# Optimization experiments

Hardware: AMD Instinct MI355X
Metric: run time of the kernel (lower is better)

The kernel has to match this reference:

```python
import jax, jax.numpy as jnp
import numpy as np

B, L = 1024, 256
POOL, FM, HEAD, EMB = 4, 64, 64, 48  # input_size=256, pool_size=4 -> 64x64 maps


def _smooth(x, scale):
    # replicate-pad box filter of width 2*scale+1, via cumsum (single pass)
    w = 2 * scale + 1
    xp = jnp.pad(x, ((0, 0), (scale, scale)), mode='edge')          # (B, L+2s)
    c = jnp.pad(jnp.cumsum(xp, axis=1), ((0, 0), (1, 0)))           # (B, L+2s+1)
    return (c[:, w:] - c[:, :-w]) / w                               # (B, L)


def _picker(g, wmap, wbias, fcw, fcb):
    # g: (B, 256, 256) pairwise feature map
    b = g.shape[0]
    p = g.reshape(b, FM, POOL, FM, POOL).mean(axis=(2, 4))          # AvgPool2d(4): (B,64,64)
    h = jax.nn.elu(jnp.einsum('bij,hij->bh', p, wmap) + wbias)      # (B, head)
    return jax.nn.elu(h @ fcw.T + fcb)                              # (B, emb)


def setup_inputs() -> dict:
    key = jax.random.key(0)
    ks = jax.random.split(key, 16)
    x = jax.random.uniform(ks[0], (B, L), dtype=jnp.float32)
    d = {'x': x}
    for i, name in enumerate(['di', 'ndi', 'dd']):
        d[f'wm_{name}'] = jax.random.normal(ks[1 + 4 * i], (HEAD, FM, FM), jnp.float32)
        d[f'b_{name}'] = jax.random.normal(ks[2 + 4 * i], (HEAD,), jnp.float32)
        d[f'fcw_{name}'] = jax.random.normal(ks[3 + 4 * i], (EMB, HEAD), jnp.float32) * (1.0 / np.sqrt(HEAD))
        d[f'fcb_{name}'] = jax.random.normal(ks[4 + 4 * i], (EMB,), jnp.float32) * 0.01
    d['fc1_w'] = jax.random.normal(ks[13], (48, 3 * EMB), jnp.float32) * (1.0 / np.sqrt(3 * EMB))
    d['fc1_b'] = jax.random.normal(ks[14], (48,), jnp.float32) * 0.01
    d['fc2_w'] = jax.random.normal(ks[15], (20, 48), jnp.float32) * (1.0 / np.sqrt(48))
    d['fc2_b'] = jnp.zeros((20,), jnp.float32)
    return d


def reference(x, wm_di, b_di, fcw_di, fcb_di,
              wm_ndi, b_ndi, fcw_ndi, fcb_ndi,
              wm_dd, b_dd, fcw_dd, fcb_dd,
              fc1_w, fc1_b, fc2_w, fc2_b):
    sm = _smooth(x, 2)
    diff = jnp.diff(sm, axis=1, prepend=x[:, :1])                   # (B, L)
    xi, xj = x[:, :, None], x[:, None, :]
    DI = xj - xi                                                    # (B, L, L)
    NDI = DI / (xj + xi + 1e-5)
    DD = diff[:, None, :] - diff[:, :, None]
    e_di = _picker(DI, wm_di, b_di, fcw_di, fcb_di)
    e_ndi = _picker(NDI, wm_ndi, b_ndi, fcw_ndi, fcb_ndi)
    e_dd = _picker(DD, wm_dd, b_dd, fcw_dd, fcb_dd)
    emb = jnp.concatenate([e_di, e_ndi, e_dd], axis=1)              # (B, 144)
    emb = jax.nn.elu(emb @ fc1_w.T + fc1_b)
    return emb @ fc2_w.T + fc2_b                                    # (B, 20)
```

## Files before the change

kernel.cpp:

```cpp
#include <hip/hip_runtime.h>
#include <hip/hip_bf16.h>
#include <math.h>

typedef __attribute__((ext_vector_type(8))) short short8;
typedef __attribute__((ext_vector_type(4))) float floatx4;

#define WS_WREDT 0u
#define WS_WMAT  (1u << 20)

__device__ __forceinline__ float eluf(float v) {
  return v > 0.f ? v : __expf(v) - 1.f;
}

__device__ __forceinline__ unsigned short f2bf(float f) {
  __hip_bfloat16 h = __float2bfloat16(f);
  return *reinterpret_cast<unsigned short*>(&h);
}

__global__ __launch_bounds__(256) void prep_kernel(
    const float* __restrict__ wm_di,
    const float* __restrict__ wm_ndi,
    const float* __restrict__ wm_dd,
    char* __restrict__ ws) {
  __shared__ float sm[64 * 65];
  const int t = threadIdx.x;
  if (blockIdx.x < 128) {
    const int sel = blockIdx.x >> 6, h = blockIdx.x & 63;
    const float* w = (sel ? wm_dd : wm_di) + h * 4096;
#pragma unroll 4
    for (int i = 0; i < 16; ++i) {
      const int e = i * 256 + t;
      sm[(e >> 6) * 65 + (e & 63)] = w[e];
    }
    __syncthreads();
    if (t < 64) {
      float cs = 0.f, rs = 0.f;
#pragma unroll 8
      for (int I = 0; I < 64; ++I) {
        cs += sm[I * 65 + t];
        rs += sm[t * 65 + I];
      }
      ((float*)(ws + WS_WREDT))[sel * 4096 + t * 64 + h] = cs - rs;
    }
  } else {
    const int h = blockIdx.x - 128;
    const float* w = wm_ndi + h * 4096;
#pragma unroll 4
    for (int i = 0; i < 16; ++i) {
      const int e = i * 256 + t;
      sm[(e >> 6) * 65 + (e & 63)] = w[e];
    }
    __syncthreads();
    const int kstep = t >> 2, kc = t & 3;
    const int lane = kc * 16 + (h & 15);
    const int n = h >> 4;
    short8 sv;
#pragma unroll
    for (int j = 0; j < 8; ++j) {
      const int k = kstep * 32 + kc * 8 + j;
      const int I = k >> 5, tt = k & 31;
      const int J = (I + 1 + tt) & 63;
      float v = 0.f;
      if (!(tt == 31 && I >= 32))
        v = 0.0625f * (sm[I * 65 + J] - sm[J * 65 + I]);
      sv[j] = (short)f2bf(v);
    }
    *(short8*)((__hip_bfloat16*)(ws + WS_WMAT) + (((n * 64 + kstep) * 64 + lane) << 3)) = sv;
  }
}

__global__ __launch_bounds__(1024, 8) void fused_kernel(
    const float* __restrict__ x,
    const float* __restrict__ b_di, const float* __restrict__ b_ndi,
    const float* __restrict__ b_dd,
    const float* __restrict__ fcw_di, const float* __restrict__ fcb_di,
    const float* __restrict__ fcw_ndi, const float* __restrict__ fcb_ndi,
    const float* __restrict__ fcw_dd, const float* __restrict__ fcb_dd,
    const float* __restrict__ fc1_w, const float* __restrict__ fc1_b,
    const float* __restrict__ fc2_w, const float* __restrict__ fc2_b,
    const char* __restrict__ ws,
    float* __restrict__ out) {
  __shared__ float xs[2][256];
  __shared__ __align__(16) unsigned short ldsA[2][2][2048];
  __shared__ float pxs[2][64], pds[2][64];
  __shared__ float hp[16][4][2][16];
  __shared__ float hh[3][2][64];
  __shared__ float emb_s[2][144];
  __shared__ float f1v_s[2][48];

  const int t = threadIdx.x;
  const int b0 = blockIdx.x * 2;
  const float* __restrict__ wredT = (const float*)(ws + WS_WREDT);
  const short* __restrict__ wmaT = (const short*)(ws + WS_WMAT);

  if (t < 512) xs[t >> 8][t & 255] = x[(b0 + (t >> 8)) * 256 + (t & 255)];
  __syncthreads();

  if (t < 128) {
    const int r = t >> 6, m = t & 63;
    const float* __restrict__ xr = xs[r];
    const int b4 = 4 * m;
    pxs[r][m] = 0.25f * (xr[b4] + xr[b4 + 1] + xr[b4 + 2] + xr[b4 + 3]);
    const int i3 = min(b4 + 4, 255), i4 = min(b4 + 5, 255);
    const float smv = 0.2f * (xr[b4 + 1] + xr[b4 + 2] + xr[b4 + 3] + xr[i3] + xr[i4]);
    float prev = __shfl_up(smv, 1, 64);
    if (m == 0) prev = xr[0];
    pds[r][m] = 0.25f * (smv - prev);
  }

#pragma unroll 1
  for (int i = 0; i < 4; ++i) {
    const int cc = t + i * 1024;
    const int r = cc >> 11, e = cc & 2047;
    const int I = e >> 5;
    const int J = (I + 1 + (e & 31)) & 63;
    const float4 xiv = *(const float4*)&xs[r][I << 2];
    const float4 xjv = *(const float4*)&xs[r][J << 2];
    const float P01 = 2.f * xjv.x * xjv.y + (xjv.x + xjv.y) * 1e-5f;
    const float P23 = 2.f * xjv.z * xjv.w + (xjv.z + xjv.w) * 1e-5f;
    const float ya[4] = {xiv.x, xiv.y, xiv.z, xiv.w};
    float s = 0.f;
#pragma unroll
    for (int a = 0; a < 4; ++a) {
      const float y = ya[a];
      const float u = y + 1e-5f;
      const float G = 2.f * y * u;
      const float D0 = (xjv.x + u) * (xjv.y + u);
      const float D1 = (xjv.z + u) * (xjv.w + u);
      s += (P01 - G) * __builtin_amdgcn_rcpf(D0);
      s += (P23 - G) * __builtin_amdgcn_rcpf(D1);
    }
    const unsigned short hi = f2bf(s);
    union { unsigned int uu; float f; } hv; hv.uu = ((unsigned int)hi) << 16;
    ldsA[0][r][e] = hi;
    ldsA[1][r][e] = f2bf(s - hv.f);
  }
  __syncthreads();

  {
    const int kh = t >> 6, lane = t & 63;
    const int arow = lane & 1;
    const int kofs = kh * 128 + ((lane >> 4) << 3);
#pragma unroll
    for (int n = 0; n < 4; ++n) {
      floatx4 acc = {0.f, 0.f, 0.f, 0.f};
#pragma unroll
      for (int s = 0; s < 4; ++s) {
        const int kk = kofs + s * 32;
        const short8 ah = *(const short8*)&ldsA[0][arow][kk];
        const short8 al = *(const short8*)&ldsA[1][arow][kk];
        const int kstep = kh * 4 + s;
        const short8 bv = *(const short8*)(wmaT + (((n * 64 + kstep) * 64 + lane) << 3));
        acc = __builtin_amdgcn_mfma_f32_16x16x32_bf16(ah, bv, acc, 0, 0, 0);
        acc = __builtin_amdgcn_mfma_f32_16x16x32_bf16(al, bv, acc, 0, 0, 0);
      }
      if (lane < 16) {
        hp[kh][n][0][lane] = acc[0];
        hp[kh][n][1][lane] = acc[1];
      }
    }
  }

  if (t < 128) {
    const int r = t >> 6, h = t & 63;
    float adi = b_di[h], add_ = b_dd[h];
#pragma unroll 8
    for (int K = 0; K < 64; ++K) {
      adi += pxs[r][K] * wredT[K * 64 + h];
      add_ += pds[r][K] * wredT[4096 + K * 64 + h];
    }
    hh[0][r][h] = eluf(adi);
    hh[2][r][h] = eluf(add_);
  }
  __syncthreads();

  if (t < 128) {
    const int row = t >> 6, h = t & 63;
    const int n = h >> 4, c = h & 15;
    float v = b_ndi[h];
#pragma unroll
    for (int kh = 0; kh < 16; ++kh) v += hp[kh][n][row][c];
    hh[1][row][h] = eluf(v);
  }
  __syncthreads();

  if (t < 2 * 144) {
    const int r = t / 144;
    const int k = t - r * 144;
    const int pick = k / 48;
    const int e = k - pick * 48;
    const float* __restrict__ fw = (pick == 0) ? fcw_di : (pick == 1) ? fcw_ndi : fcw_dd;
    const float* __restrict__ fb = (pick == 0) ? fcb_di : (pick == 1) ? fcb_ndi : fcb_dd;
    float a = fb[e];
#pragma unroll 8
    for (int hq = 0; hq < 64; ++hq) a += hh[pick][r][hq] * fw[e * 64 + hq];
    emb_s[r][k] = eluf(a);
  }
  __syncthreads();

  if (t < 2 * 48) {
    const int r = t / 48, o = t - (t / 48) * 48;
    float a = fc1_b[o];
#pragma unroll 8
    for (int k = 0; k < 144; ++k) a += emb_s[r][k] * fc1_w[o * 144 + k];
    f1v_s[r][o] = eluf(a);
  }
  __syncthreads();

  if (t < 2 * 20) {
    const int r = t / 20, o = t - (t / 20) * 20;
    float a = fc2_b[o];
#pragma unroll
    for (int j = 0; j < 48; ++j) a += f1v_s[r][j] * fc2_w[o * 48 + j];
    out[(b0 + r) * 20 + o] = a;
  }
}

extern "C" void kernel_launch(void* const* d_in, const int* in_sizes, int n_in,
                              void* d_out, int out_size, void* d_ws, size_t ws_size,
                              hipStream_t stream) {
  const float* x       = (const float*)d_in[0];
  const float* wm_di   = (const float*)d_in[1];
  const float* b_di    = (const float*)d_in[2];
  const float* fcw_di  = (const float*)d_in[3];
  const float* fcb_di  = (const float*)d_in[4];
  const float* wm_ndi  = (const float*)d_in[5];
  const float* b_ndi   = (const float*)d_in[6];
  const float* fcw_ndi = (const float*)d_in[7];
  const float* fcb_ndi = (const float*)d_in[8];
  const float* wm_dd   = (const float*)d_in[9];
  const float* b_dd    = (const float*)d_in[10];
  const float* fcw_dd  = (const float*)d_in[11];
  const float* fcb_dd  = (const float*)d_in[12];
  const float* fc1_w   = (const float*)d_in[13];
  const float* fc1_b   = (const float*)d_in[14];
  const float* fc2_w   = (const float*)d_in[15];
  const float* fc2_b   = (const float*)d_in[16];
  float* out = (float*)d_out;
  char* ws = (char*)d_ws;

  prep_kernel<<<192, 256, 0, stream>>>(wm_di, wm_ndi, wm_dd, ws);
  fused_kernel<<<512, 1024, 0, stream>>>(
      x, b_di, b_ndi, b_dd,
      fcw_di, fcb_di, fcw_ndi, fcb_ndi, fcw_dd, fcb_dd,
      fc1_w, fc1_b, fc2_w, fc2_b, ws, out);
}
```

Before: 27.04 us.

## Fuse weight prep into main kernel with per-group flag synchronization

```diff
diff --git a/kernel.cpp b/kernel.cpp
--- a/kernel.cpp
+++ b/kernel.cpp
@@ -5,8 +5,9 @@
 typedef __attribute__((ext_vector_type(8))) short short8;
 typedef __attribute__((ext_vector_type(4))) float floatx4;
 
-#define WS_WREDT 0u
-#define WS_WMAT  (1u << 20)
+#define MAGIC 0x5EEDBEEFu
+#define WS_CLASS(g) ((size_t)(1 + (g)) << 20)
+#define WMA_OFF (512u << 10)
 
 __device__ __forceinline__ float eluf(float v) {
   return v > 0.f ? v : __expf(v) - 1.f;
@@ -17,60 +18,11 @@
   return *reinterpret_cast<unsigned short*>(&h);
 }
 
-__global__ __launch_bounds__(256) void prep_kernel(
+__global__ __launch_bounds__(1024, 8) void mono_kernel(
+    const float* __restrict__ x,
     const float* __restrict__ wm_di,
     const float* __restrict__ wm_ndi,
     const float* __restrict__ wm_dd,
-    char* __restrict__ ws) {
-  __shared__ float sm[64 * 65];
-  const int t = threadIdx.x;
-  if (blockIdx.x < 128) {
-    const int sel = blockIdx.x >> 6, h = blockIdx.x & 63;
-    const float* w = (sel ? wm_dd : wm_di) + h * 4096;
-#pragma unroll 4
-    for (int i = 0; i < 16; ++i) {
-      const int e = i * 256 + t;
-      sm[(e >> 6) * 65 + (e & 63)] = w[e];
-    }
-    __syncthreads();
-    if (t < 64) {
-      float cs = 0.f, rs = 0.f;
-#pragma unroll 8
-      for (int I = 0; I < 64; ++I) {
-        cs += sm[I * 65 + t];
-        rs += sm[t * 65 + I];
-      }
-      ((float*)(ws + WS_WREDT))[sel * 4096 + t * 64 + h] = cs - rs;
-    }
-  } else {
-    const int h = blockIdx.x - 128;
-    const float* w = wm_ndi + h * 4096;
-#pragma unroll 4
-    for (int i = 0; i < 16; ++i) {
-      const int e = i * 256 + t;
-      sm[(e >> 6) * 65 + (e & 63)] = w[e];
-    }
-    __syncthreads();
-    const int kstep = t >> 2, kc = t & 3;
-    const int lane = kc * 16 + (h & 15);
-    const int n = h >> 4;
-    short8 sv;
-#pragma unroll
-    for (int j = 0; j < 8; ++j) {
-      const int k = kstep * 32 + kc * 8 + j;
-      const int I = k >> 5, tt = k & 31;
-      const int J = (I + 1 + tt) & 63;
-      float v = 0.f;
-      if (!(tt == 31 && I >= 32))
-        v = 0.0625f * (sm[I * 65 + J] - sm[J * 65 + I]);
-      sv[j] = (short)f2bf(v);
-    }
-    *(short8*)((__hip_bfloat16*)(ws + WS_WMAT) + (((n * 64 + kstep) * 64 + lane) << 3)) = sv;
-  }
-}
-
-__global__ __launch_bounds__(1024, 8) void fused_kernel(
-    const float* __restrict__ x,
     const float* __restrict__ b_di, const float* __restrict__ b_ndi,
     const float* __restrict__ b_dd,
     const float* __restrict__ fcw_di, const float* __restrict__ fcb_di,
@@ -78,10 +30,13 @@
     const float* __restrict__ fcw_dd, const float* __restrict__ fcb_dd,
     const float* __restrict__ fc1_w, const float* __restrict__ fc1_b,
     const float* __restrict__ fc2_w, const float* __restrict__ fc2_b,
-    const char* __restrict__ ws,
+    char* __restrict__ ws,
     float* __restrict__ out) {
   __shared__ float xs[2][256];
-  __shared__ __align__(16) unsigned short ldsA[2][2][2048];
+  __shared__ __align__(16) union {
+    unsigned short ldsA[2][2][2048];
+    float sm[64 * 65];
+  } sh;
   __shared__ float pxs[2][64], pds[2][64];
   __shared__ float hp[16][4][2][16];
   __shared__ float hh[3][2][64];
@@ -89,12 +44,71 @@
   __shared__ float f1v_s[2][48];
 
   const int t = threadIdx.x;
-  const int b0 = blockIdx.x * 2;
-  const float* __restrict__ wredT = (const float*)(ws + WS_WREDT);
-  const short* __restrict__ wmaT = (const short*)(ws + WS_WMAT);
+  const int bid = blockIdx.x;
+  const int b0 = bid * 2;
+  const int g = bid & 7, uu = bid >> 3;
+
+  unsigned* __restrict__ flags = (unsigned*)ws;
+  float* __restrict__ wredT_c = (float*)(ws + WS_CLASS(g));
+  __hip_bfloat16* __restrict__ wmaT_c = (__hip_bfloat16*)(ws + WS_CLASS(g) + WMA_OFF);
 
   if (t < 512) xs[t >> 8][t & 255] = x[(b0 + (t >> 8)) * 256 + (t & 255)];
   __syncthreads();
+
+  if (uu < 24) {
+#pragma unroll 1
+    for (int q = 0; q < 8; ++q) {
+      const int hu = uu * 8 + q;
+      const float* __restrict__ w = (hu < 64)  ? wm_di + hu * 4096
+                                  : (hu < 128) ? wm_dd + (hu - 64) * 4096
+                                               : wm_ndi + (hu - 128) * 4096;
+#pragma unroll
+      for (int i = 0; i < 4; ++i) {
+        const int e = i * 1024 + t;
+        sh.sm[(e >> 6) * 65 + (e & 63)] = w[e];
+      }
+      __syncthreads();
+      if (hu < 128) {
+        const int sel = hu >> 6, h = hu & 63;
+        const int K = t >> 4, part = t & 15;
+        float a = 0.f;
+#pragma unroll
+        for (int ii = 0; ii < 4; ++ii) {
+          const int I = part * 4 + ii;
+          a += sh.sm[I * 65 + K] - sh.sm[K * 65 + I];
+        }
+        a += __shfl_xor(a, 1, 64);
+        a += __shfl_xor(a, 2, 64);
+        a += __shfl_xor(a, 4, 64);
+        a += __shfl_xor(a, 8, 64);
+        if (part == 0) wredT_c[sel * 4096 + K * 64 + h] = a;
+      } else {
+        const int h = hu - 128;
+        if (t < 256) {
+          const int kstep = t >> 2, kc = t & 3;
+          const int lane2 = kc * 16 + (h & 15);
+          const int n = h >> 4;
+          short8 sv;
+#pragma unroll
+          for (int j = 0; j < 8; ++j) {
+            const int k = kstep * 32 + kc * 8 + j;
+            const int I = k >> 5, tt2 = k & 31;
+            const int J = (I + 1 + tt2) & 63;
+            float v = 0.f;
+            if (!(tt2 == 31 && I >= 32))
+              v = 0.0625f * (sh.sm[I * 65 + J] - sh.sm[J * 65 + I]);
+            sv[j] = (short)f2bf(v);
+          }
+          *(short8*)(wmaT_c + (((n * 64 + kstep) * 64 + lane2) << 3)) = sv;
+        }
+      }
+      __syncthreads();
+    }
+    __threadfence();
+    if (t == 0)
+      __hip_atomic_store(&flags[g * 32 + uu], MAGIC, __ATOMIC_RELEASE,
+                         __HIP_MEMORY_SCOPE_AGENT);
+  }
 
   if (t < 128) {
     const int r = t >> 6, m = t & 63;
@@ -123,32 +137,48 @@
 #pragma unroll
     for (int a = 0; a < 4; ++a) {
       const float y = ya[a];
-      const float u = y + 1e-5f;
-      const float G = 2.f * y * u;
-      const float D0 = (xjv.x + u) * (xjv.y + u);
-      const float D1 = (xjv.z + u) * (xjv.w + u);
+      const float u2 = y + 1e-5f;
+      const float G = 2.f * y * u2;
+      const float D0 = (xjv.x + u2) * (xjv.y + u2);
+      const float D1 = (xjv.z + u2) * (xjv.w + u2);
       s += (P01 - G) * __builtin_amdgcn_rcpf(D0);
       s += (P23 - G) * __builtin_amdgcn_rcpf(D1);
     }
     const unsigned short hi = f2bf(s);
-    union { unsigned int uu; float f; } hv; hv.uu = ((unsigned int)hi) << 16;
-    ldsA[0][r][e] = hi;
-    ldsA[1][r][e] = f2bf(s - hv.f);
-  }
-  __syncthreads();
+    union { unsigned int ub; float f; } hv; hv.ub = ((unsigned int)hi) << 16;
+    sh.ldsA[0][r][e] = hi;
+    sh.ldsA[1][r][e] = f2bf(s - hv.f);
+  }
+
+  {
+    const int lane = t & 63;
+    if (t < 64) {
+      int iters = 0;
+      bool ok;
+      do {
+        unsigned f = MAGIC;
+        if (lane < 24)
+          f = __hip_atomic_load(&flags[g * 32 + lane], __ATOMIC_ACQUIRE,
+                                __HIP_MEMORY_SCOPE_AGENT);
+        ok = __all(f == MAGIC);
+      } while (!ok && ++iters < (1 << 22));
+    }
+    __syncthreads();
+  }
 
   {
     const int kh = t >> 6, lane = t & 63;
     const int arow = lane & 1;
     const int kofs = kh * 128 + ((lane >> 4) << 3);
+    const short* __restrict__ wmaT = (const short*)wmaT_c;
 #pragma unroll
     for (int n = 0; n < 4; ++n) {
       floatx4 acc = {0.f, 0.f, 0.f, 0.f};
 #pragma unroll
       for (int s = 0; s < 4; ++s) {
         const int kk = kofs + s * 32;
-        const short8 ah = *(const short8*)&ldsA[0][arow][kk];
-        const short8 al = *(const short8*)&ldsA[1][arow][kk];
+        const short8 ah = *(const short8*)&sh.ldsA[0][arow][kk];
+        const short8 al = *(const short8*)&sh.ldsA[1][arow][kk];
         const int kstep = kh * 4 + s;
         const short8 bv = *(const short8*)(wmaT + (((n * 64 + kstep) * 64 + lane) << 3));
         acc = __builtin_amdgcn_mfma_f32_16x16x32_bf16(ah, bv, acc, 0, 0, 0);
@@ -166,8 +196,8 @@
     float adi = b_di[h], add_ = b_dd[h];
 #pragma unroll 8
     for (int K = 0; K < 64; ++K) {
-      adi += pxs[r][K] * wredT[K * 64 + h];
-      add_ += pds[r][K] * wredT[4096 + K * 64 + h];
+      adi += pxs[r][K] * wredT_c[K * 64 + h];
+      add_ += pds[r][K] * wredT_c[4096 + K * 64 + h];
     }
     hh[0][r][h] = eluf(adi);
     hh[2][r][h] = eluf(add_);
@@ -239,9 +269,8 @@
   float* out = (float*)d_out;
   char* ws = (char*)d_ws;
 
-  prep_kernel<<<192, 256, 0, stream>>>(wm_di, wm_ndi, wm_dd, ws);
-  fused_kernel<<<512, 1024, 0, stream>>>(
-      x, b_di, b_ndi, b_dd,
+  mono_kernel<<<512, 1024, 0, stream>>>(
+      x, wm_di, wm_ndi, wm_dd, b_di, b_ndi, b_dd,
       fcw_di, fcb_di, fcw_ndi, fcb_ndi, fcw_dd, fcb_dd,
       fc1_w, fc1_b, fc2_w, fc2_b, ws, out);
 }
```

Result: slower. 80.45 us (+197.5%).
